# Kernel tuning notes

Measured on AMD Instinct MI355X. Metric: run time of the kernel, lower is better.

The kernel has to match this reference:

```python
import jax, jax.numpy as jnp
import numpy as np

N_NODES = 50000
N_EDGES = 800000
IN_DIM = 128
HEADS = 4
CH = 64
NEG_SLOPE = 0.2


def _gat_conv(x, src, dst, W, a_src, a_dst, bias):
    """PyG-style GATConv (self-loops already appended to src/dst).
    x: [N, F_in], W: [F_in, H*C], a_src/a_dst: [H, C], bias: [H*C]."""
    n = x.shape[0]
    h = (x @ W).reshape(n, HEADS, CH)                      # [N, H, C]
    alpha_s = (h * a_src).sum(-1)                          # [N, H]
    alpha_d = (h * a_dst).sum(-1)                          # [N, H]
    e = jax.nn.leaky_relu(alpha_s[src] + alpha_d[dst], NEG_SLOPE)  # [E, H]
    m = jax.ops.segment_max(e, dst, num_segments=n)        # segment softmax over dst
    e = jnp.exp(e - m[dst])
    denom = jax.ops.segment_sum(e, dst, num_segments=n)
    alpha = e / (denom[dst] + 1e-16)                       # [E, H]
    out = jax.ops.segment_sum(h[src] * alpha[:, :, None], dst, num_segments=n)
    return out.reshape(n, HEADS * CH) + bias               # concat=True


def setup_inputs() -> dict:
    key = jax.random.key(0)
    ks = jax.random.split(key, 10)
    x = jax.random.normal(ks[0], (N_NODES, IN_DIM), dtype=jnp.float32)
    edge_index = jax.random.randint(ks[1], (2, N_EDGES), 0, N_NODES, dtype=jnp.int64)
    s1 = 1.0 / np.sqrt(IN_DIM)
    s2 = 1.0 / np.sqrt(HEADS * CH)
    return {
        "x": x,
        "edge_index": edge_index,
        "W1": jax.random.normal(ks[2], (IN_DIM, HEADS * CH), dtype=jnp.float32) * s1,
        "a_src1": jax.random.normal(ks[3], (HEADS, CH), dtype=jnp.float32) * s1,
        "a_dst1": jax.random.normal(ks[4], (HEADS, CH), dtype=jnp.float32) * s1,
        "b1": jnp.zeros((HEADS * CH,), dtype=jnp.float32),
        "W2": jax.random.normal(ks[5], (HEADS * CH, HEADS * CH), dtype=jnp.float32) * s2,
        "a_src2": jax.random.normal(ks[6], (HEADS, CH), dtype=jnp.float32) * s2,
        "a_dst2": jax.random.normal(ks[7], (HEADS, CH), dtype=jnp.float32) * s2,
        "b2": jnp.zeros((HEADS * CH,), dtype=jnp.float32),
        "fc_w": jax.random.normal(ks[8], (HEADS * CH, 1), dtype=jnp.float32) * s2,
        "fc_b": jnp.zeros((1,), dtype=jnp.float32),
    }


def reference(x, edge_index, W1, a_src1, a_dst1, b1, W2, a_src2, a_dst2, b2, fc_w, fc_b):
    n = x.shape[0]
    loop = jnp.arange(n, dtype=edge_index.dtype)           # PyG GATConv adds self-loops
    src = jnp.concatenate([edge_index[0], loop])
    dst = jnp.concatenate([edge_index[1], loop])
    h = jax.nn.elu(_gat_conv(x, src, dst, W1, a_src1, a_dst1, b1))
    h = jax.nn.elu(_gat_conv(h, src, dst, W2, a_src2, a_dst2, b2))
    return jax.nn.sigmoid(h @ fc_w + fc_b)                 # [N, 1]
```

## Files before the change

### kernel.cpp

```cpp
#include <hip/hip_runtime.h>
#include <hip/hip_bf16.h>

#define N_NODES 50000
#define N_EDGES 800000
#define NCHUNK 256
#define EPC 3125
#define NBUCKET 196
#define SCAN_N 50176
#define SCAN_BLOCKS 196

typedef __attribute__((ext_vector_type(8))) short bf16x8;
typedef __attribute__((ext_vector_type(4))) float f32x4;
typedef __attribute__((ext_vector_type(2))) float f32x2;
typedef unsigned short ushort_t;

__device__ __forceinline__ float bf2f(unsigned short u) {
    union { unsigned u32; float f; } v; v.u32 = (unsigned)u << 16; return v.f;
}
__device__ __forceinline__ unsigned short f2bf(float f) {
    __hip_bfloat16 h = __float2bfloat16(f);
    return *reinterpret_cast<unsigned short*>(&h);
}
__device__ __forceinline__ f32x2 bfpair(unsigned u) {
    union { unsigned a; float f; } lo, hi;
    lo.a = u << 16;
    hi.a = u & 0xFFFF0000u;
    f32x2 r; r.x = lo.f; r.y = hi.f; return r;
}
__device__ __forceinline__ void pkfma(f32x2& d, f32x2 a, f32x2 b) {
    asm("v_pk_fma_f32 %0, %1, %2, %0" : "+v"(d) : "v"(a), "v"(b));
}
__device__ __forceinline__ void gload16(const void* src, void* lds) {
    __builtin_amdgcn_global_load_lds(
        (const __attribute__((address_space(1))) unsigned int*)src,
        (__attribute__((address_space(3))) unsigned int*)lds, 16, 0, 0);
}

__device__ __forceinline__ int detect_is32_block(const unsigned* __restrict__ w,
                                                 int* s_is32, int tid) {
    if (tid == 0) {
        unsigned o = 0;
#pragma unroll
        for (int k = 1; k < 32; k += 2) o |= w[k];
        *s_is32 = (o != 0u);
    }
    __syncthreads();
    return *s_is32;
}

__device__ __forceinline__ int edge_elem(const unsigned* __restrict__ w, int is32, long long idx) {
    return is32 ? (int)w[idx] : (int)w[2 * idx];
}

__global__ void __launch_bounds__(256) bucket_hist_kernel(const unsigned* __restrict__ ew,
                                                          int* __restrict__ chunkHist) {
    __shared__ int s_is32;
    __shared__ int hist[NBUCKET];
    int t = threadIdx.x, b = blockIdx.x;
    int is32 = detect_is32_block(ew, &s_is32, t);
    for (int k = t; k < NBUCKET; k += 256) hist[k] = 0;
    __syncthreads();
    long long e0 = (long long)b * EPC;
    for (int k = t; k < EPC; k += 256) {
        int d = edge_elem(ew, is32, (long long)N_EDGES + e0 + k);
        atomicAdd(&hist[d >> 8], 1);
    }
    __syncthreads();
    for (int k = t; k < NBUCKET; k += 256)
        chunkHist[k * NCHUNK + b] = hist[k];
}

__global__ void __launch_bounds__(256) scan1_kernel(const int* __restrict__ in,
                                                    int* __restrict__ excl, int* __restrict__ bsum) {
    __shared__ int s[256];
    int b = blockIdx.x, t = threadIdx.x, i = b * 256 + t;
    int v = in[i];
    s[t] = v;
    __syncthreads();
    for (int off = 1; off < 256; off <<= 1) {
        int y = (t >= off) ? s[t - off] : 0;
        __syncthreads();
        s[t] += y;
        __syncthreads();
    }
    excl[i] = s[t] - v;
    if (t == 255) bsum[b] = s[255];
}

__global__ void __launch_bounds__(256) scan2_kernel(const int* __restrict__ bsum,
                                                    int* __restrict__ boff) {
    __shared__ int s[256];
    int t = threadIdx.x;
    int v = (t < SCAN_BLOCKS) ? bsum[t] : 0;
    s[t] = v;
    __syncthreads();
    for (int off = 1; off < 256; off <<= 1) {
        int y = (t >= off) ? s[t - off] : 0;
        __syncthreads();
        s[t] += y;
        __syncthreads();
    }
    if (t < SCAN_BLOCKS) boff[t] = s[t] - v;
}

__global__ void __launch_bounds__(256) scan3_kernel(const int* __restrict__ boff,
                                                    int* __restrict__ excl) {
    int i = blockIdx.x * 256 + threadIdx.x;
    excl[i] += boff[blockIdx.x];
}

__global__ void __launch_bounds__(256) bucket_scatter_kernel(const unsigned* __restrict__ ew,
                                                             const int* __restrict__ chunkOff,
                                                             unsigned* __restrict__ ebuf) {
    __shared__ int s_is32;
    __shared__ int cur[NBUCKET];
    int t = threadIdx.x, b = blockIdx.x;
    int is32 = detect_is32_block(ew, &s_is32, t);
    for (int k = t; k < NBUCKET; k += 256) cur[k] = chunkOff[k * NCHUNK + b];
    __syncthreads();
    long long e0 = (long long)b * EPC;
    for (int k = t; k < EPC; k += 256) {
        long long e = e0 + k;
        unsigned s = (unsigned)edge_elem(ew, is32, e);
        int d = edge_elem(ew, is32, (long long)N_EDGES + e);
        int pos = atomicAdd(&cur[d >> 8], 1);
        ebuf[pos] = s | ((unsigned)d << 16);
    }
}

__global__ void __launch_bounds__(256) bucket_sort_kernel(const unsigned* __restrict__ ebuf,
                                                          const int* __restrict__ chunkOff,
                                                          unsigned* __restrict__ edge_csr,
                                                          int* __restrict__ row_ptr) {
    __shared__ int cnt[256];
    __shared__ int s[256];
    int b = blockIdx.x, t = threadIdx.x;
    int start = chunkOff[b * NCHUNK];
    int end = (b + 1 < NBUCKET) ? chunkOff[(b + 1) * NCHUNK] : N_EDGES;
    cnt[t] = 0;
    __syncthreads();
    for (int e = start + t; e < end; e += 256) {
        int d = (int)(ebuf[e] >> 16);
        atomicAdd(&cnt[d & 255], 1);
    }
    __syncthreads();
    s[t] = cnt[t];
    __syncthreads();
    for (int off = 1; off < 256; off <<= 1) {
        int y = (t >= off) ? s[t - off] : 0;
        __syncthreads();
        s[t] += y;
        __syncthreads();
    }
    int excl = s[t] - cnt[t];
    int node = b * 256 + t;
    if (node <= N_NODES) row_ptr[node] = start + excl;
    cnt[t] = start + excl;
    __syncthreads();
    for (int e = start + t; e < end; e += 256) {
        unsigned pk = ebuf[e];
        int pos = atomicAdd(&cnt[(pk >> 16) & 255], 1);
        edge_csr[pos] = pk;
    }
}

#define CONV_BLOCKS 6250
__global__ void __launch_bounds__(256) prep_kernel(const float* __restrict__ x,
                                                   ushort_t* __restrict__ xbf,
                                                   const float* __restrict__ W1,
                                                   ushort_t* __restrict__ W1t,
                                                   const float* __restrict__ W2,
                                                   ushort_t* __restrict__ W2t) {
    int b = blockIdx.x, t = threadIdx.x;
    if (b < CONV_BLOCKS) {
        int i = b * 256 + t;
        float4 v = ((const float4*)x)[i];
        ushort4 o;
        o.x = f2bf(v.x); o.y = f2bf(v.y); o.z = f2bf(v.z); o.w = f2bf(v.w);
        ((ushort4*)xbf)[i] = o;
    } else if (b < CONV_BLOCKS + 128) {
        int id = (b - CONV_BLOCKS) * 256 + t;
        int n = id >> 7, k = id & 127;
        W1t[id] = f2bf(W1[k * 256 + n]);
    } else {
        int id = (b - CONV_BLOCKS - 128) * 256 + t;
        int n = id >> 8, k = id & 255;
        W2t[id] = f2bf(W2[k * 256 + n]);
    }
}

template <int K>
__global__ void __launch_bounds__(256) mfma_gemm_kernel(const ushort_t* __restrict__ A,
                                                        const ushort_t* __restrict__ Wt,
                                                        void* __restrict__ Cv, int M,
                                                        const float* __restrict__ a_src,
                                                        const float* __restrict__ a_dst,
                                                        float* __restrict__ alpha_s,
                                                        float* __restrict__ alpha_d) {
    constexpr int CPR = K / 8;
    constexpr int NT = K / 64;
    __shared__ ushort_t Bs[64 * K];
    __shared__ ushort_t As[2][64 * 64];
    __shared__ float ps[64][2], pd[64][2];

    int tid = threadIdx.x;
    int wave = tid >> 6, lane = tid & 63;
    int l15 = lane & 15, l4 = lane >> 4;
    int wr = wave >> 1, wc = wave & 1;
    int colblock = blockIdx.x;
    int rowblock = blockIdx.y;

    for (int base = 0; base < 64 * CPR; base += 256) {
        int p = base + wave * 64 + lane;
        int row = p / CPR;
        int cs = p % CPR;
        int c = cs ^ (row & 7);
        const ushort_t* src = Wt + (long long)(colblock * 64 + row) * K + c * 8;
        void* dst = ((char*)Bs) + (base + wave * 64) * 16;
        gload16(src, dst);
    }
    {
        int r = lane >> 3, cs = lane & 7;
        int c = cs ^ r;
#pragma unroll
        for (int q = 0; q < 2; ++q) {
            int lrow = wave * 16 + q * 8;
            int grow = rowblock * 64 + lrow + r;
            if (grow >= M) grow = M - 1;
            const ushort_t* src = A + (long long)grow * K + c * 8;
            void* dst = ((char*)&As[0][0]) + lrow * 128;
            gload16(src, dst);
        }
    }
    __syncthreads();

    f32x4 acc[2][2] = {};
#pragma unroll
    for (int t = 0; t < NT; ++t) {
        if (t + 1 < NT) {
            int r = lane >> 3, cs = lane & 7;
            int c = cs ^ r;
#pragma unroll
            for (int q = 0; q < 2; ++q) {
                int lrow = wave * 16 + q * 8;
                int grow = rowblock * 64 + lrow + r;
                if (grow >= M) grow = M - 1;
                const ushort_t* src = A + (long long)grow * K + (t + 1) * 64 + c * 8;
                void* dst = ((char*)&As[(t + 1) & 1][0]) + lrow * 128;
                gload16(src, dst);
            }
        }
        const ushort_t* At = &As[t & 1][0];
#pragma unroll
        for (int w = 0; w < 2; ++w) {
            bf16x8 a[2], b[2];
#pragma unroll
            for (int mi = 0; mi < 2; ++mi) {
                int row = wr * 32 + mi * 16 + l15;
                int slot = (w * 4 + l4) ^ (l15 & 7);
                a[mi] = *(const bf16x8*)&At[row * 64 + slot * 8];
            }
#pragma unroll
            for (int ni = 0; ni < 2; ++ni) {
                int brow = wc * 32 + ni * 16 + l15;
                int slot = (t * 8 + w * 4 + l4) ^ (l15 & 7);
                b[ni] = *(const bf16x8*)&Bs[brow * CPR * 8 + slot * 8];
            }
#pragma unroll
            for (int mi = 0; mi < 2; ++mi)
#pragma unroll
                for (int ni = 0; ni < 2; ++ni)
                    acc[mi][ni] = __builtin_amdgcn_mfma_f32_16x16x32_bf16(a[mi], b[ni],
                                                                          acc[mi][ni], 0, 0, 0);
        }
        __syncthreads();
    }

    {
        float as0 = a_src[colblock * 64 + wc * 32 + l15];
        float as1 = a_src[colblock * 64 + wc * 32 + 16 + l15];
        float ad0 = a_dst[colblock * 64 + wc * 32 + l15];
        float ad1 = a_dst[colblock * 64 + wc * 32 + 16 + l15];
#pragma unroll
        for (int mi = 0; mi < 2; ++mi)
#pragma unroll
            for (int q = 0; q < 4; ++q) {
                float sv = acc[mi][0][q] * as0 + acc[mi][1][q] * as1;
                float dv = acc[mi][0][q] * ad0 + acc[mi][1][q] * ad1;
#pragma unroll
                for (int w = 1; w < 16; w <<= 1) {
                    sv += __shfl_xor(sv, w, 64);
                    dv += __shfl_xor(dv, w, 64);
                }
                if (l15 == 0) {
                    int row = wr * 32 + mi * 16 + l4 * 4 + q;
                    ps[row][wc] = sv;
                    pd[row][wc] = dv;
                }
            }
    }

    ushort_t* ep = ((ushort_t*)&As[0][0]) + wave * 1280;
#pragma unroll
    for (int mi = 0; mi < 2; ++mi)
#pragma unroll
        for (int ni = 0; ni < 2; ++ni)
#pragma unroll
            for (int q = 0; q < 4; ++q) {
                int row = mi * 16 + l4 * 4 + q;
                int col = ni * 16 + l15;
                ep[row * 40 + col] = f2bf(acc[mi][ni][q]);
            }
    __syncthreads();
#pragma unroll
    for (int j = 0; j < 2; ++j) {
        int p = lane * 2 + j;
        int row = p >> 2, seg = p & 3;
        uint4 v = *(const uint4*)&ep[row * 40 + seg * 8];
        int grow = rowblock * 64 + wr * 32 + row;
        int gcol = colblock * 64 + wc * 32 + seg * 8;
        if (grow < M) {
            f32x2 f01 = bfpair(v.x), f23 = bfpair(v.y);
            f32x2 f45 = bfpair(v.z), f67 = bfpair(v.w);
            int d0 = 0, d1 = 0;
            d0 = __builtin_amdgcn_cvt_pk_fp8_f32(f01.x, f01.y, d0, false);
            d0 = __builtin_amdgcn_cvt_pk_fp8_f32(f23.x, f23.y, d0, true);
            d1 = __builtin_amdgcn_cvt_pk_fp8_f32(f45.x, f45.y, d1, false);
            d1 = __builtin_amdgcn_cvt_pk_fp8_f32(f67.x, f67.y, d1, true);
            uint2 o; o.x = (unsigned)d0; o.y = (unsigned)d1;
            *(uint2*)((char*)Cv + (long long)grow * 256 + gcol) = o;
        }
    }
    if (tid < 64) {
        int ga = rowblock * 64 + tid;
        if (ga < M) {
            alpha_s[ga * 4 + colblock] = ps[tid][0] + ps[tid][1];
            alpha_d[ga * 4 + colblock] = pd[tid][0] + pd[tid][1];
        }
    }
}

template <int LAYER>
__global__ void __launch_bounds__(256) aggregate_kernel(
    const void* __restrict__ gv, const float* __restrict__ alpha_s,
    const float* __restrict__ alpha_d, const int* __restrict__ row_ptr,
    const unsigned* __restrict__ edge_csr,
    const float* __restrict__ bias, ushort_t* __restrict__ out_bf,
    const float* __restrict__ fc_w, const float* __restrict__ fc_b,
    float* __restrict__ final_out) {
    int wave = threadIdx.x >> 6;
    int lane = threadIdx.x & 63;
    int i = blockIdx.x * 4 + wave;
    int hd = lane >> 4;
    const char* gb = (const char*)gv;
    unsigned loff = (unsigned)(lane << 2);

    float ad = alpha_d[i * 4 + hd];
    float e0 = alpha_s[i * 4 + hd] + ad;
    e0 = e0 > 0.f ? e0 : 0.2f * e0;
    float w0 = __expf(e0);
    f32x2 wp0; wp0.x = w0; wp0.y = w0;
    f32x2 acc01 = {0.f, 0.f}, acc23 = {0.f, 0.f};
    {
        unsigned sv = *(const unsigned*)(gb + (((unsigned)i << 8) | loff));
        pkfma(acc01, wp0, __builtin_amdgcn_cvt_pk_f32_fp8(sv, false));
        pkfma(acc23, wp0, __builtin_amdgcn_cvt_pk_f32_fp8(sv, true));
    }
    float wsum = w0;

    int p = row_ptr[i], p1 = row_ptr[i + 1];
    for (; p + 8 <= p1; p += 8) {
        int j[8]; float as[8]; unsigned hh[8];
#pragma unroll
        for (int u = 0; u < 8; ++u) j[u] = (int)(edge_csr[p + u] & 0xFFFFu);
#pragma unroll
        for (int u = 0; u < 8; ++u) as[u] = alpha_s[j[u] * 4 + hd];
#pragma unroll
        for (int u = 0; u < 8; ++u)
            hh[u] = *(const unsigned*)(gb + (((unsigned)j[u] << 8) | loff));
#pragma unroll
        for (int u = 0; u < 8; ++u) {
            float e = as[u] + ad;
            e = e > 0.f ? e : 0.2f * e;
            float wt = __expf(e);
            wsum += wt;
            f32x2 wp; wp.x = wt; wp.y = wt;
            pkfma(acc01, wp, __builtin_amdgcn_cvt_pk_f32_fp8(hh[u], false));
            pkfma(acc23, wp, __builtin_amdgcn_cvt_pk_f32_fp8(hh[u], true));
        }
    }
    for (; p < p1; ++p) {
        int j = (int)(edge_csr[p] & 0xFFFFu);
        float e = alpha_s[j * 4 + hd] + ad;
        e = e > 0.f ? e : 0.2f * e;
        float wt = __expf(e);
        unsigned hj = *(const unsigned*)(gb + (((unsigned)j << 8) | loff));
        wsum += wt;
        f32x2 wp; wp.x = wt; wp.y = wt;
        pkfma(acc01, wp, __builtin_amdgcn_cvt_pk_f32_fp8(hj, false));
        pkfma(acc23, wp, __builtin_amdgcn_cvt_pk_f32_fp8(hj, true));
    }
    float inv = 1.f / (wsum + 1e-16f);
    int c = lane * 4;
    float4 b4 = *(const float4*)&bias[c];
    float o0 = acc01.x * inv + b4.x;
    float o1 = acc01.y * inv + b4.y;
    float o2 = acc23.x * inv + b4.z;
    float o3 = acc23.y * inv + b4.w;
    o0 = o0 > 0.f ? o0 : __expf(o0) - 1.f;
    o1 = o1 > 0.f ? o1 : __expf(o1) - 1.f;
    o2 = o2 > 0.f ? o2 : __expf(o2) - 1.f;
    o3 = o3 > 0.f ? o3 : __expf(o3) - 1.f;
    if (LAYER == 1) {
        ushort4 o;
        o.x = f2bf(o0); o.y = f2bf(o1); o.z = f2bf(o2); o.w = f2bf(o3);
        ((ushort4*)out_bf)[(long long)i * 64 + lane] = o;
    } else {
        float4 fw = *(const float4*)&fc_w[c];
        float dot = o0 * fw.x + o1 * fw.y + o2 * fw.z + o3 * fw.w;
#pragma unroll
        for (int off = 32; off; off >>= 1) dot += __shfl_down(dot, off, 64);
        if (lane == 0) final_out[i] = 1.f / (1.f + __expf(-(dot + fc_b[0])));
    }
}

extern "C" void kernel_launch(void* const* d_in, const int* in_sizes, int n_in,
                              void* d_out, int out_size, void* d_ws, size_t ws_size,
                              hipStream_t stream) {
    const float* x   = (const float*)d_in[0];
    const unsigned* ei = (const unsigned*)d_in[1];
    const float* W1  = (const float*)d_in[2];
    const float* as1 = (const float*)d_in[3];
    const float* ad1 = (const float*)d_in[4];
    const float* b1  = (const float*)d_in[5];
    const float* W2  = (const float*)d_in[6];
    const float* as2 = (const float*)d_in[7];
    const float* ad2 = (const float*)d_in[8];
    const float* b2  = (const float*)d_in[9];
    const float* fcw = (const float*)d_in[10];
    const float* fcb = (const float*)d_in[11];

    char* ws = (char*)d_ws;
    void* g1f8         = (void*)(ws + 0);
    void* g2f8         = (void*)(ws + 12800000);
    ushort_t* hactbf   = (ushort_t*)(ws + 25600000);
    ushort_t* xbf      = (ushort_t*)(ws + 51200000);
    ushort_t* W1t      = (ushort_t*)(ws + 64000000);
    ushort_t* W2t      = (ushort_t*)(ws + 64100000);
    float* asv         = (float*)(ws + 64300000);
    float* adv         = (float*)(ws + 65100000);
    int* row_ptr       = (int*)(ws + 65900000);
    int* chunkHist     = (int*)(ws + 66110000);
    int* chunkOff      = (int*)(ws + 66320000);
    unsigned* ebuf     = (unsigned*)(ws + 66530000);
    unsigned* edge_csr = (unsigned*)(ws + 69730000);
    int* bsum          = (int*)(ws + 72930000);
    int* boff          = (int*)(ws + 72931024);

    prep_kernel<<<CONV_BLOCKS + 128 + 256, 256, 0, stream>>>(x, xbf, W1, W1t, W2, W2t);

    bucket_hist_kernel<<<NCHUNK, 256, 0, stream>>>(ei, chunkHist);
    scan1_kernel<<<SCAN_BLOCKS, 256, 0, stream>>>(chunkHist, chunkOff, bsum);
    scan2_kernel<<<1, 256, 0, stream>>>(bsum, boff);
    scan3_kernel<<<SCAN_BLOCKS, 256, 0, stream>>>(boff, chunkOff);
    bucket_scatter_kernel<<<NCHUNK, 256, 0, stream>>>(ei, chunkOff, ebuf);
    bucket_sort_kernel<<<NBUCKET, 256, 0, stream>>>(ebuf, chunkOff, edge_csr, row_ptr);

    mfma_gemm_kernel<128><<<dim3(4, (N_NODES + 63) / 64), 256, 0, stream>>>(
        xbf, W1t, g1f8, N_NODES, as1, ad1, asv, adv);
    aggregate_kernel<1><<<N_NODES / 4, 256, 0, stream>>>(g1f8, asv, adv, row_ptr, edge_csr,
                                                         b1, hactbf, nullptr, nullptr, nullptr);
    mfma_gemm_kernel<256><<<dim3(4, (N_NODES + 63) / 64), 256, 0, stream>>>(
        hactbf, W2t, g2f8, N_NODES, as2, ad2, asv, adv);
    aggregate_kernel<2><<<N_NODES / 4, 256, 0, stream>>>(g2f8, asv, adv, row_ptr, edge_csr,
                                                         b2, nullptr, fcw, fcb, (float*)d_out);
}
```

Measured before the change: 187.4 us.

## Sort nodes by degree for balanced aggregation and fuse histogram into prep

Builds a degree histogram during the bucket sort, scans it, and scatters node ids into a degree-sorted permutation, so that the waves in each aggregate block handle nodes of similar degree and there is less intra-block imbalance. The edge bucket histogram is also merged into the prep kernel to save a launch, and the row pointers are made wave-uniform with readfirstlane. The cost is a memset plus two extra small kernels, and outputs are now written in permuted node order, which scatters the writes.

```diff
diff --git a/kernel.cpp b/kernel.cpp
--- a/kernel.cpp
+++ b/kernel.cpp
@@ -52,125 +52,16 @@
     return is32 ? (int)w[idx] : (int)w[2 * idx];
 }
 
-__global__ void __launch_bounds__(256) bucket_hist_kernel(const unsigned* __restrict__ ew,
-                                                          int* __restrict__ chunkHist) {
-    __shared__ int s_is32;
-    __shared__ int hist[NBUCKET];
-    int t = threadIdx.x, b = blockIdx.x;
-    int is32 = detect_is32_block(ew, &s_is32, t);
-    for (int k = t; k < NBUCKET; k += 256) hist[k] = 0;
-    __syncthreads();
-    long long e0 = (long long)b * EPC;
-    for (int k = t; k < EPC; k += 256) {
-        int d = edge_elem(ew, is32, (long long)N_EDGES + e0 + k);
-        atomicAdd(&hist[d >> 8], 1);
-    }
-    __syncthreads();
-    for (int k = t; k < NBUCKET; k += 256)
-        chunkHist[k * NCHUNK + b] = hist[k];
-}
-
-__global__ void __launch_bounds__(256) scan1_kernel(const int* __restrict__ in,
-                                                    int* __restrict__ excl, int* __restrict__ bsum) {
-    __shared__ int s[256];
-    int b = blockIdx.x, t = threadIdx.x, i = b * 256 + t;
-    int v = in[i];
-    s[t] = v;
-    __syncthreads();
-    for (int off = 1; off < 256; off <<= 1) {
-        int y = (t >= off) ? s[t - off] : 0;
-        __syncthreads();
-        s[t] += y;
-        __syncthreads();
-    }
-    excl[i] = s[t] - v;
-    if (t == 255) bsum[b] = s[255];
-}
-
-__global__ void __launch_bounds__(256) scan2_kernel(const int* __restrict__ bsum,
-                                                    int* __restrict__ boff) {
-    __shared__ int s[256];
-    int t = threadIdx.x;
-    int v = (t < SCAN_BLOCKS) ? bsum[t] : 0;
-    s[t] = v;
-    __syncthreads();
-    for (int off = 1; off < 256; off <<= 1) {
-        int y = (t >= off) ? s[t - off] : 0;
-        __syncthreads();
-        s[t] += y;
-        __syncthreads();
-    }
-    if (t < SCAN_BLOCKS) boff[t] = s[t] - v;
-}
-
-__global__ void __launch_bounds__(256) scan3_kernel(const int* __restrict__ boff,
-                                                    int* __restrict__ excl) {
-    int i = blockIdx.x * 256 + threadIdx.x;
-    excl[i] += boff[blockIdx.x];
-}
-
-__global__ void __launch_bounds__(256) bucket_scatter_kernel(const unsigned* __restrict__ ew,
-                                                             const int* __restrict__ chunkOff,
-                                                             unsigned* __restrict__ ebuf) {
-    __shared__ int s_is32;
-    __shared__ int cur[NBUCKET];
-    int t = threadIdx.x, b = blockIdx.x;
-    int is32 = detect_is32_block(ew, &s_is32, t);
-    for (int k = t; k < NBUCKET; k += 256) cur[k] = chunkOff[k * NCHUNK + b];
-    __syncthreads();
-    long long e0 = (long long)b * EPC;
-    for (int k = t; k < EPC; k += 256) {
-        long long e = e0 + k;
-        unsigned s = (unsigned)edge_elem(ew, is32, e);
-        int d = edge_elem(ew, is32, (long long)N_EDGES + e);
-        int pos = atomicAdd(&cur[d >> 8], 1);
-        ebuf[pos] = s | ((unsigned)d << 16);
-    }
-}
-
-__global__ void __launch_bounds__(256) bucket_sort_kernel(const unsigned* __restrict__ ebuf,
-                                                          const int* __restrict__ chunkOff,
-                                                          unsigned* __restrict__ edge_csr,
-                                                          int* __restrict__ row_ptr) {
-    __shared__ int cnt[256];
-    __shared__ int s[256];
-    int b = blockIdx.x, t = threadIdx.x;
-    int start = chunkOff[b * NCHUNK];
-    int end = (b + 1 < NBUCKET) ? chunkOff[(b + 1) * NCHUNK] : N_EDGES;
-    cnt[t] = 0;
-    __syncthreads();
-    for (int e = start + t; e < end; e += 256) {
-        int d = (int)(ebuf[e] >> 16);
-        atomicAdd(&cnt[d & 255], 1);
-    }
-    __syncthreads();
-    s[t] = cnt[t];
-    __syncthreads();
-    for (int off = 1; off < 256; off <<= 1) {
-        int y = (t >= off) ? s[t - off] : 0;
-        __syncthreads();
-        s[t] += y;
-        __syncthreads();
-    }
-    int excl = s[t] - cnt[t];
-    int node = b * 256 + t;
-    if (node <= N_NODES) row_ptr[node] = start + excl;
-    cnt[t] = start + excl;
-    __syncthreads();
-    for (int e = start + t; e < end; e += 256) {
-        unsigned pk = ebuf[e];
-        int pos = atomicAdd(&cnt[(pk >> 16) & 255], 1);
-        edge_csr[pos] = pk;
-    }
-}
-
 #define CONV_BLOCKS 6250
+#define PREP_W_BLOCKS (CONV_BLOCKS + 128 + 256)
 __global__ void __launch_bounds__(256) prep_kernel(const float* __restrict__ x,
                                                    ushort_t* __restrict__ xbf,
                                                    const float* __restrict__ W1,
                                                    ushort_t* __restrict__ W1t,
                                                    const float* __restrict__ W2,
-                                                   ushort_t* __restrict__ W2t) {
+                                                   ushort_t* __restrict__ W2t,
+                                                   const unsigned* __restrict__ ew,
+                                                   int* __restrict__ chunkHist) {
     int b = blockIdx.x, t = threadIdx.x;
     if (b < CONV_BLOCKS) {
         int i = b * 256 + t;
@@ -182,10 +73,163 @@
         int id = (b - CONV_BLOCKS) * 256 + t;
         int n = id >> 7, k = id & 127;
         W1t[id] = f2bf(W1[k * 256 + n]);
-    } else {
+    } else if (b < CONV_BLOCKS + 128 + 256) {
         int id = (b - CONV_BLOCKS - 128) * 256 + t;
         int n = id >> 8, k = id & 255;
         W2t[id] = f2bf(W2[k * 256 + n]);
+    } else {
+        __shared__ int s_is32;
+        __shared__ int hist[NBUCKET];
+        int c = b - PREP_W_BLOCKS;
+        int is32 = detect_is32_block(ew, &s_is32, t);
+        for (int k = t; k < NBUCKET; k += 256) hist[k] = 0;
+        __syncthreads();
+        long long e0 = (long long)c * EPC;
+        for (int k = t; k < EPC; k += 256) {
+            int d = edge_elem(ew, is32, (long long)N_EDGES + e0 + k);
+            atomicAdd(&hist[d >> 8], 1);
+        }
+        __syncthreads();
+        for (int k = t; k < NBUCKET; k += 256)
+            chunkHist[k * NCHUNK + c] = hist[k];
+    }
+}
+
+__global__ void __launch_bounds__(256) scan1_kernel(const int* __restrict__ in,
+                                                    int* __restrict__ excl, int* __restrict__ bsum) {
+    __shared__ int s[256];
+    int b = blockIdx.x, t = threadIdx.x, i = b * 256 + t;
+    int v = in[i];
+    s[t] = v;
+    __syncthreads();
+    for (int off = 1; off < 256; off <<= 1) {
+        int y = (t >= off) ? s[t - off] : 0;
+        __syncthreads();
+        s[t] += y;
+        __syncthreads();
+    }
+    excl[i] = s[t] - v;
+    if (t == 255) bsum[b] = s[255];
+}
+
+__global__ void __launch_bounds__(256) scan2_kernel(const int* __restrict__ bsum,
+                                                    int* __restrict__ boff) {
+    __shared__ int s[256];
+    int t = threadIdx.x;
+    int v = (t < SCAN_BLOCKS) ? bsum[t] : 0;
+    s[t] = v;
+    __syncthreads();
+    for (int off = 1; off < 256; off <<= 1) {
+        int y = (t >= off) ? s[t - off] : 0;
+        __syncthreads();
+        s[t] += y;
+        __syncthreads();
+    }
+    if (t < SCAN_BLOCKS) boff[t] = s[t] - v;
+}
+
+__global__ void __launch_bounds__(256) scan3_kernel(const int* __restrict__ boff,
+                                                    int* __restrict__ excl) {
+    int i = blockIdx.x * 256 + threadIdx.x;
+    excl[i] += boff[blockIdx.x];
+}
+
+__global__ void __launch_bounds__(256) bucket_scatter_kernel(const unsigned* __restrict__ ew,
+                                                             const int* __restrict__ chunkOff,
+                                                             unsigned* __restrict__ ebuf) {
+    __shared__ int s_is32;
+    __shared__ int cur[NBUCKET];
+    int t = threadIdx.x, b = blockIdx.x;
+    int is32 = detect_is32_block(ew, &s_is32, t);
+    for (int k = t; k < NBUCKET; k += 256) cur[k] = chunkOff[k * NCHUNK + b];
+    __syncthreads();
+    long long e0 = (long long)b * EPC;
+    for (int k = t; k < EPC; k += 256) {
+        long long e = e0 + k;
+        unsigned s = (unsigned)edge_elem(ew, is32, e);
+        int d = edge_elem(ew, is32, (long long)N_EDGES + e);
+        int pos = atomicAdd(&cur[d >> 8], 1);
+        ebuf[pos] = s | ((unsigned)d << 16);
+    }
+}
+
+__global__ void __launch_bounds__(256) bucket_sort_kernel(const unsigned* __restrict__ ebuf,
+                                                          const int* __restrict__ chunkOff,
+                                                          unsigned* __restrict__ edge_csr,
+                                                          int* __restrict__ row_ptr,
+                                                          int* __restrict__ dhist) {
+    __shared__ int cnt[256];
+    __shared__ int s[256];
+    __shared__ int dh[64];
+    int b = blockIdx.x, t = threadIdx.x;
+    int start = chunkOff[b * NCHUNK];
+    int end = (b + 1 < NBUCKET) ? chunkOff[(b + 1) * NCHUNK] : N_EDGES;
+    cnt[t] = 0;
+    if (t < 64) dh[t] = 0;
+    __syncthreads();
+    for (int e = start + t; e < end; e += 256) {
+        int d = (int)(ebuf[e] >> 16);
+        atomicAdd(&cnt[d & 255], 1);
+    }
+    __syncthreads();
+    int node = b * 256 + t;
+    int mydeg = cnt[t];
+    if (node < N_NODES) atomicAdd(&dh[mydeg < 63 ? mydeg : 63], 1);
+    s[t] = mydeg;
+    __syncthreads();
+    for (int off = 1; off < 256; off <<= 1) {
+        int y = (t >= off) ? s[t - off] : 0;
+        __syncthreads();
+        s[t] += y;
+        __syncthreads();
+    }
+    int excl = s[t] - mydeg;
+    if (node <= N_NODES) row_ptr[node] = start + excl;
+    cnt[t] = start + excl;
+    __syncthreads();
+    for (int e = start + t; e < end; e += 256) {
+        unsigned pk = ebuf[e];
+        int pos = atomicAdd(&cnt[(pk >> 16) & 255], 1);
+        edge_csr[pos] = pk;
+    }
+    if (t < 64 && dh[t]) atomicAdd(&dhist[t], dh[t]);
+}
+
+__global__ void __launch_bounds__(64) dscan_kernel(const int* __restrict__ dhist,
+                                                   int* __restrict__ dcur) {
+    int t = threadIdx.x;
+    int v = dhist[t];
+    int sum = v;
+#pragma unroll
+    for (int off = 1; off < 64; off <<= 1) {
+        int y = __shfl_up(sum, off, 64);
+        if (t >= off) sum += y;
+    }
+    dcur[t] = sum - v;
+}
+
+__global__ void __launch_bounds__(256) dscatter_kernel(const int* __restrict__ row_ptr,
+                                                       int* __restrict__ dcur,
+                                                       int* __restrict__ perm) {
+    __shared__ int lh[64], lbase[64];
+    int t = threadIdx.x, i = blockIdx.x * 256 + t;
+    if (t < 64) lh[t] = 0;
+    __syncthreads();
+    int deg = 0;
+    if (i < N_NODES) {
+        deg = row_ptr[i + 1] - row_ptr[i];
+        if (deg > 63) deg = 63;
+        atomicAdd(&lh[deg], 1);
+    }
+    __syncthreads();
+    if (t < 64) {
+        lbase[t] = lh[t] ? atomicAdd(&dcur[t], lh[t]) : 0;
+        lh[t] = 0;
+    }
+    __syncthreads();
+    if (i < N_NODES) {
+        int rank = atomicAdd(&lh[deg], 1);
+        perm[lbase[deg] + rank] = i;
     }
 }
 
@@ -344,13 +388,13 @@
 __global__ void __launch_bounds__(256) aggregate_kernel(
     const void* __restrict__ gv, const float* __restrict__ alpha_s,
     const float* __restrict__ alpha_d, const int* __restrict__ row_ptr,
-    const unsigned* __restrict__ edge_csr,
+    const unsigned* __restrict__ edge_csr, const int* __restrict__ perm,
     const float* __restrict__ bias, ushort_t* __restrict__ out_bf,
     const float* __restrict__ fc_w, const float* __restrict__ fc_b,
     float* __restrict__ final_out) {
     int wave = threadIdx.x >> 6;
     int lane = threadIdx.x & 63;
-    int i = blockIdx.x * 4 + wave;
+    int i = __builtin_amdgcn_readfirstlane(perm[blockIdx.x * 4 + wave]);
     int hd = lane >> 4;
     const char* gb = (const char*)gv;
     unsigned loff = (unsigned)(lane << 2);
@@ -368,11 +412,13 @@
     }
     float wsum = w0;
 
-    int p = row_ptr[i], p1 = row_ptr[i + 1];
+    int p = __builtin_amdgcn_readfirstlane(row_ptr[i]);
+    int p1 = __builtin_amdgcn_readfirstlane(row_ptr[i + 1]);
     for (; p + 8 <= p1; p += 8) {
         int j[8]; float as[8]; unsigned hh[8];
 #pragma unroll
-        for (int u = 0; u < 8; ++u) j[u] = (int)(edge_csr[p + u] & 0xFFFFu);
+        for (int u = 0; u < 8; ++u)
+            j[u] = (int)(edge_csr[p + u] & 0xFFFFu);
 #pragma unroll
         for (int u = 0; u < 8; ++u) as[u] = alpha_s[j[u] * 4 + hd];
 #pragma unroll
@@ -454,24 +500,30 @@
     int* chunkOff      = (int*)(ws + 66320000);
     unsigned* ebuf     = (unsigned*)(ws + 66530000);
     unsigned* edge_csr = (unsigned*)(ws + 69730000);
-    int* bsum          = (int*)(ws + 72930000);
-    int* boff          = (int*)(ws + 72931024);
-
-    prep_kernel<<<CONV_BLOCKS + 128 + 256, 256, 0, stream>>>(x, xbf, W1, W1t, W2, W2t);
-
-    bucket_hist_kernel<<<NCHUNK, 256, 0, stream>>>(ei, chunkHist);
+    int* perm          = (int*)(ws + 72930000);
+    int* bsum          = (int*)(ws + 73130000);
+    int* boff          = (int*)(ws + 73131024);
+    int* dhist         = (int*)(ws + 73132048);
+    int* dcur          = (int*)(ws + 73132304);
+
+    hipMemsetAsync(dhist, 0, 64 * 4, stream);
+
+    prep_kernel<<<PREP_W_BLOCKS + NCHUNK, 256, 0, stream>>>(x, xbf, W1, W1t, W2, W2t,
+                                                            ei, chunkHist);
     scan1_kernel<<<SCAN_BLOCKS, 256, 0, stream>>>(chunkHist, chunkOff, bsum);
     scan2_kernel<<<1, 256, 0, stream>>>(bsum, boff);
     scan3_kernel<<<SCAN_BLOCKS, 256, 0, stream>>>(boff, chunkOff);
     bucket_scatter_kernel<<<NCHUNK, 256, 0, stream>>>(ei, chunkOff, ebuf);
-    bucket_sort_kernel<<<NBUCKET, 256, 0, stream>>>(ebuf, chunkOff, edge_csr, row_ptr);
+    bucket_sort_kernel<<<NBUCKET, 256, 0, stream>>>(ebuf, chunkOff, edge_csr, row_ptr, dhist);
+    dscan_kernel<<<1, 64, 0, stream>>>(dhist, dcur);
+    dscatter_kernel<<<SCAN_BLOCKS, 256, 0, stream>>>(row_ptr, dcur, perm);
 
     mfma_gemm_kernel<128><<<dim3(4, (N_NODES + 63) / 64), 256, 0, stream>>>(
         xbf, W1t, g1f8, N_NODES, as1, ad1, asv, adv);
-    aggregate_kernel<1><<<N_NODES / 4, 256, 0, stream>>>(g1f8, asv, adv, row_ptr, edge_csr,
+    aggregate_kernel<1><<<N_NODES / 4, 256, 0, stream>>>(g1f8, asv, adv, row_ptr, edge_csr, perm,
                                                          b1, hactbf, nullptr, nullptr, nullptr);
     mfma_gemm_kernel<256><<<dim3(4, (N_NODES + 63) / 64), 256, 0, stream>>>(
         hactbf, W2t, g2f8, N_NODES, as2, ad2, asv, adv);
-    aggregate_kernel<2><<<N_NODES / 4, 256, 0, stream>>>(g2f8, asv, adv, row_ptr, edge_csr,
+    aggregate_kernel<2><<<N_NODES / 4, 256, 0, stream>>>(g2f8, asv, adv, row_ptr, edge_csr, perm,
                                                          b2, nullptr, fcw, fcb, (float*)d_out);
 }
```

Result: no change. 185.9 us (-0.8%).
